# Kernel tuning notes

Measured on AMD Instinct MI355X. Metric: run time of the kernel, lower is better.

The kernel has to match this reference:

```python
import jax, jax.numpy as jnp
import numpy as np

B, S, H = 2, 2048, 3584
NH, NKV, HD = 28, 4, 128
GROUPS = NH // NKV  # 7
SCALING = HD ** -0.5
NEG = -1e9


def setup_inputs() -> dict:
    key = jax.random.key(0)
    ks = jax.random.split(key, 10)
    hidden_states = jax.random.normal(ks[0], (B, S, H), jnp.float32)
    # RoPE tables (faithful functional form; use real rotary angles)
    inv_freq = 1.0 / (1000000.0 ** (jnp.arange(0, HD, 2, dtype=jnp.float32) / HD))
    pos = jnp.arange(S, dtype=jnp.float32)
    freqs = jnp.outer(pos, inv_freq)                 # [S, HD/2]
    emb = jnp.concatenate([freqs, freqs], axis=-1)   # [S, HD]
    cos = jnp.broadcast_to(jnp.cos(emb)[None], (B, S, HD))
    sin = jnp.broadcast_to(jnp.sin(emb)[None], (B, S, HD))
    # additive causal mask [1,1,S,S]
    causal = jnp.tril(jnp.ones((S, S), dtype=bool))
    attention_mask = jnp.where(causal, 0.0, NEG).astype(jnp.float32)[None, None]
    sc = 0.02
    Wq = jax.random.normal(ks[1], (NH * HD, H), jnp.float32) * sc
    bq = jax.random.normal(ks[2], (NH * HD,), jnp.float32) * sc
    Wk = jax.random.normal(ks[3], (NKV * HD, H), jnp.float32) * sc
    bk = jax.random.normal(ks[4], (NKV * HD,), jnp.float32) * sc
    Wv = jax.random.normal(ks[5], (NKV * HD, H), jnp.float32) * sc
    bv = jax.random.normal(ks[6], (NKV * HD,), jnp.float32) * sc
    Wo = jax.random.normal(ks[7], (H, NH * HD), jnp.float32) * sc
    return dict(hidden_states=hidden_states, cos=cos, sin=sin,
                attention_mask=attention_mask, Wq=Wq, bq=bq, Wk=Wk, bk=bk,
                Wv=Wv, bv=bv, Wo=Wo)


def _rotate_half(x):
    x1, x2 = jnp.split(x, 2, axis=-1)
    return jnp.concatenate([-x2, x1], axis=-1)


def reference(hidden_states, cos, sin, attention_mask, Wq, bq, Wk, bk, Wv, bv, Wo):
    Bv_, Sv_ = hidden_states.shape[:2]
    # projections -> [B, heads, S, HD]
    q = (hidden_states @ Wq.T + bq).reshape(Bv_, Sv_, NH, HD).transpose(0, 2, 1, 3)
    k = (hidden_states @ Wk.T + bk).reshape(Bv_, Sv_, NKV, HD).transpose(0, 2, 1, 3)
    v = (hidden_states @ Wv.T + bv).reshape(Bv_, Sv_, NKV, HD).transpose(0, 2, 1, 3)
    # RoPE (unsqueeze_dim=1)
    c, s = cos[:, None], sin[:, None]
    q = q * c + _rotate_half(q) * s
    k = k * c + _rotate_half(k) * s
    # repeat_kv for GQA
    k = jnp.repeat(k, GROUPS, axis=1)  # [B, NH, S, HD]
    v = jnp.repeat(v, GROUPS, axis=1)
    scores = jnp.einsum('bhqd,bhkd->bhqk', q, k) * SCALING
    scores = scores + attention_mask[:, :, :, :k.shape[-2]]
    probs = jax.nn.softmax(scores.astype(jnp.float32), axis=-1).astype(q.dtype)
    attn = jnp.einsum('bhqk,bhkd->bhqd', probs, v)          # [B, NH, S, HD]
    attn = attn.transpose(0, 2, 1, 3).reshape(Bv_, Sv_, NH * HD)
    out = attn @ Wo.T
    return out, probs
```

## Files before the change

kernel.cpp:

```cpp
#include <hip/hip_runtime.h>

#define Bn 2
#define Sn 2048
#define Hn 3584
#define NHn 28
#define NKVn 4
#define HDn 128
#define GROUPSn 7
#define SCALEF 0.08838834764831845f
#define SCALE2F (0.08838834764831845f * 1.4426950408889634f)
#define NOUT 14680064LL

typedef __attribute__((ext_vector_type(4))) float f4v;
typedef __attribute__((ext_vector_type(16))) float f32x16;
typedef __attribute__((ext_vector_type(8))) short bf16x8;
typedef __attribute__((ext_vector_type(4))) short s16x4;

typedef __attribute__((address_space(1))) void gvoid;
typedef __attribute__((address_space(3))) void lvoid;
#define GLL16(g, l) __builtin_amdgcn_global_load_lds((gvoid*)(void*)(g), (lvoid*)(l), 16, 0, 0)

__device__ __forceinline__ short f2bf(float f) {
  unsigned u = __builtin_bit_cast(unsigned, f);
  u = (u + 0x7fffu + ((u >> 16) & 1u)) >> 16;
  return (short)u;
}

__global__ __launch_bounds__(256) void cast_bf16(const float* __restrict__ in,
                                                 short* __restrict__ out, long long n4) {
  long long i = (long long)blockIdx.x * 256 + threadIdx.x;
  long long stride = (long long)gridDim.x * 256;
  for (; i < n4; i += stride) {
    f4v f = ((const f4v*)in)[i];
    s16x4 o = { f2bf(f.x), f2bf(f.y), f2bf(f.z), f2bf(f.w) };
    ((s16x4*)out)[i] = o;
  }
}

__global__ __launch_bounds__(256) void cast_weights(const float* __restrict__ Wq,
                                                    const float* __restrict__ Wk,
                                                    const float* __restrict__ Wv,
                                                    const float* __restrict__ Wo,
                                                    short* __restrict__ wqkv_bf,
                                                    short* __restrict__ wo_bf) {
  long long i = (long long)blockIdx.x * 256 + threadIdx.x;
  long long stride = (long long)gridDim.x * 256;
  for (; i < 7340032LL; i += stride) {
    const f4v* src;
    s16x4* dst;
    if (i < 3211264LL) {
      src = (const f4v*)Wq + i;             dst = (s16x4*)wqkv_bf + i;
    } else if (i < 3670016LL) {
      src = (const f4v*)Wk + (i - 3211264); dst = (s16x4*)(wqkv_bf + 12845056LL) + (i - 3211264);
    } else if (i < 4128768LL) {
      src = (const f4v*)Wv + (i - 3670016); dst = (s16x4*)(wqkv_bf + 14680064LL) + (i - 3670016);
    } else {
      src = (const f4v*)Wo + (i - 4128768); dst = (s16x4*)wo_bf + (i - 4128768);
    }
    f4v f = *src;
    s16x4 o = { f2bf(f.x), f2bf(f.y), f2bf(f.z), f2bf(f.w) };
    *dst = o;
  }
}

__global__ __launch_bounds__(256) void concat_bias(const float* __restrict__ bq,
                                                   const float* __restrict__ bk,
                                                   const float* __restrict__ bv,
                                                   float* __restrict__ out) {
  int i = blockIdx.x * 256 + threadIdx.x;
  if (i < 3584) out[i] = bq[i];
  else if (i < 4096) out[i] = bk[i - 3584];
  else if (i < 4608) out[i] = bv[i - 4096];
}

__device__ __forceinline__ void mm128x64_core(const short* __restrict__ Atile, long long lda,
                                              const short* __restrict__ Btile, long long ldb,
                                              int nk, short* lA, short* lB, f4v (&acc)[4][4]) {
  const int tid = threadIdx.x;
  const int lane = tid & 63;
  const int wr = (tid >> 6) >> 1, wc = (tid >> 6) & 1;
  const int fr = lane & 15;
  const int g = lane >> 4;
  int rsw[4], csw[4];
#pragma unroll
  for (int i = 0; i < 4; ++i) {
    int M = i * 256 + tid;
    rsw[i] = M >> 3;
    csw[i] = (M & 7) ^ (rsw[i] & 7);
  }
  for (int kt = 0; kt < nk; ++kt) {
#pragma unroll
    for (int i = 0; i < 4; ++i) {
      GLL16(Atile + (long long)rsw[i] * lda + kt * 64 + csw[i] * 8, lA + (i * 256 + tid) * 8);
      GLL16(Btile + (long long)rsw[i] * ldb + kt * 64 + csw[i] * 8, lB + (i * 256 + tid) * 8);
    }
    __syncthreads();
#pragma unroll
    for (int kk = 0; kk < 2; ++kk) {
      bf16x8 af[4], bf[4];
#pragma unroll
      for (int m = 0; m < 4; ++m) {
        int r = wr * 64 + m * 16 + fr;
        af[m] = *(const bf16x8*)&lA[r * 64 + ((kk * 4 + g) ^ (r & 7)) * 8];
      }
#pragma unroll
      for (int n = 0; n < 4; ++n) {
        int r = wc * 64 + n * 16 + fr;
        bf[n] = *(const bf16x8*)&lB[r * 64 + ((kk * 4 + g) ^ (r & 7)) * 8];
      }
#pragma unroll
      for (int m = 0; m < 4; ++m)
#pragma unroll
        for (int n = 0; n < 4; ++n)
          acc[m][n] = __builtin_amdgcn_mfma_f32_16x16x32_bf16(af[m], bf[n], acc[m][n], 0, 0, 0);
    }
    __syncthreads();
  }
}

__global__ __launch_bounds__(256) void gemm_persist(const short* __restrict__ A,
                                                    const short* __restrict__ B,
                                                    float* __restrict__ C,
                                                    const float* __restrict__ bias,
                                                    int K, int N, int gx, int ntiles) {
  __shared__ alignas(16) short lA[8192];
  __shared__ alignas(16) short lB[8192];
  const int nt8 = ntiles >> 3;
  const int lane = threadIdx.x & 63;
  const int wr = (threadIdx.x >> 6) >> 1, wc = (threadIdx.x >> 6) & 1;
  const int rr = (lane >> 4) * 4, cc = lane & 15;
  for (int vt = blockIdx.x; vt < ntiles; vt += gridDim.x) {
    const int tile = (vt & 7) * nt8 + (vt >> 3);
    const int bx = tile % gx, by = tile / gx;
    const long long brow = (long long)by * 128;
    const long long bcol = (long long)bx * 128;
    f4v acc[4][4] = {};
    mm128x64_core(A + brow * K, K, B + bcol * K, K, K >> 6, lA, lB, acc);
#pragma unroll
    for (int n = 0; n < 4; ++n) {
      long long col = bcol + wc * 64 + n * 16 + cc;
      float bv = bias ? bias[col] : 0.f;
#pragma unroll
      for (int m = 0; m < 4; ++m) {
#pragma unroll
        for (int j = 0; j < 4; ++j) {
          long long row = brow + wr * 64 + m * 16 + rr + j;
          C[row * N + col] = acc[m][n][j] + bv;
        }
      }
    }
  }
}

__global__ __launch_bounds__(256) void rope_qk(const float* __restrict__ qkv,
                                               const float* __restrict__ cosb,
                                               const float* __restrict__ sinb,
                                               short* __restrict__ qo,
                                               short* __restrict__ ko) {
  long long bs = blockIdx.x;
  int b = (int)(bs >> 11);
  int s = (int)(bs & 2047);
  const float* row = qkv + bs * 4608;
  const float* cp = cosb + bs * 128;
  const float* sp = sinb + bs * 128;
  for (int i = threadIdx.x; i < 4096; i += 256) {
    int d = i & 127;
    float c = cp[d], sn = sp[d];
    float x = row[i];
    float xr = (d < 64) ? -row[i + 64] : row[i - 64];
    short v = f2bf(x * c + xr * sn);
    if (i < 3584) {
      int h = i >> 7;
      qo[(((long long)(b * NHn + h) * Sn + s)) * HDn + d] = v;
    } else {
      int h = (i - 3584) >> 7;
      ko[(((long long)(b * NKVn + h) * Sn + s)) * HDn + d] = v;
    }
  }
}

__global__ void vtrans(const float* __restrict__ qkv, short* __restrict__ vt) {
  __shared__ float tile[32][33];
  int bh = blockIdx.z;
  int b = bh >> 2, h = bh & 3;
  int s0 = blockIdx.x * 32, d0 = blockIdx.y * 32;
  int tx = threadIdx.x, ty = threadIdx.y;
#pragma unroll
  for (int j = 0; j < 32; j += 8) {
    int s = s0 + ty + j;
    tile[ty + j][tx] = qkv[((long long)(b * Sn + s)) * 4608 + 4096 + h * 128 + d0 + tx];
  }
  __syncthreads();
#pragma unroll
  for (int j = 0; j < 32; j += 8) {
    int d = d0 + ty + j;
    vt[((long long)(bh * 128 + d)) * Sn + s0 + tx] = f2bf(tile[tx][ty + j]);
  }
}

__global__ __launch_bounds__(256, 1) void fused_attn7(const short* __restrict__ Q,
                                                      const short* __restrict__ Kb,
                                                      const short* __restrict__ Vt,
                                                      float* __restrict__ probs,
                                                      short* __restrict__ attn) {
  __shared__ alignas(16) short lK[2][8192];
  __shared__ alignas(16) short lV[8192];
  const int tid = threadIdx.x;
  const int w = tid >> 6;
  const int lane = tid & 63;
  const int lam = lane & 31, h = lane >> 5;
  const int qb = 15 - (int)blockIdx.x;
  const int bh = blockIdx.y;
  const int b = bh / NHn, hh = bh - b * NHn, kv = hh / GROUPSn;
  const short* Qb = Q + (long long)bh * (Sn * HDn);
  const short* Kbb = Kb + (long long)(b * NKVn + kv) * (Sn * HDn);
  const short* Vb = Vt + (long long)(b * NKVn + kv) * (HDn * Sn);
  float* Pb = probs + (long long)bh * ((long long)Sn * Sn) + (long long)qb * 128 * Sn;
  const int qloc = w * 32 + lam;

  bf16x8 qf[8];
  {
    const short* qr = Qb + (long long)(qb * 128 + qloc) * HDn + h * 8;
#pragma unroll
    for (int s = 0; s < 8; ++s) qf[s] = *(const bf16x8*)(qr + s * 16);
  }
  int rswK[4], cswK[4];
#pragma unroll
  for (int i = 0; i < 4; ++i) {
    int M = i * 256 + tid;
    rswK[i] = M >> 4;
    cswK[i] = (M & 15) ^ (rswK[i] & 15);
  }
  int rswV[4], cswV[4];
#pragma unroll
  for (int i = 0; i < 4; ++i) {
    int M = i * 256 + tid;
    rswV[i] = M >> 3;
    cswV[i] = (M & 7) ^ (rswV[i] & 7);
  }
  const int c8 = lam & 15;
  const int v8 = lam & 7;
  const int nkt = 2 * qb + 2;

#define STAGEK(BUF, KT) do {                                                      \
    const short* base_ = Kbb + (long long)(KT) * 64 * HDn;                        \
    _Pragma("unroll")                                                             \
    for (int i = 0; i < 4; ++i)                                                   \
      GLL16(base_ + (long long)rswK[i] * HDn + cswK[i] * 8,                       \
            (short*)lK[BUF] + (i * 256 + tid) * 8);                               \
  } while (0)

#define STAGEV(KT) do {                                                           \
    _Pragma("unroll")                                                             \
    for (int i = 0; i < 4; ++i)                                                   \
      GLL16(Vb + (long long)rswV[i] * Sn + (KT) * 64 + cswV[i] * 8,               \
            lV + (i * 256 + tid) * 8);                                            \
  } while (0)

#define QKT2(ACCP, LCUR) do {                                                     \
    __builtin_amdgcn_s_setprio(1);                                                \
    _Pragma("unroll")                                                             \
    for (int s = 0; s < 8; ++s) {                                                 \
      const int co_ = ((s * 2 + h) ^ c8) * 8;                                     \
      _Pragma("unroll")                                                           \
      for (int a = 0; a < 2; ++a) {                                               \
        bf16x8 kf_ = *(const bf16x8*)&(LCUR)[(a * 32 + lam) * 128 + co_];         \
        ACCP[a] = __builtin_amdgcn_mfma_f32_32x32x16_bf16(kf_, qf[s], ACCP[a], 0, 0, 0); \
      }                                                                           \
    }                                                                             \
    __builtin_amdgcn_s_setprio(0);                                                \
  } while (0)

  float lsum = 0.f;
  STAGEK(0, 0);
  int cur = 0;
  for (int kt = 0; kt < nkt; ++kt) {
    __syncthreads();
    if (kt + 1 < nkt) STAGEK(cur ^ 1, kt + 1);
    const short* lcur = (const short*)lK[cur];
    f32x16 accp[2] = {};
    QKT2(accp, lcur);
    const int kbase = kt * 64 - qb * 128;
#pragma unroll
    for (int a = 0; a < 2; ++a)
#pragma unroll
      for (int r = 0; r < 16; ++r) {
        int kloc = a * 32 + (r & 3) + 8 * (r >> 2) + 4 * h;
        float s = fminf(accp[a][r] * SCALE2F, 86.5f);
        float p = exp2f(s);
        if (kbase + kloc > qloc) p = 0.f;
        lsum += p;
      }
    cur ^= 1;
  }
  lsum += __shfl_xor(lsum, 32);
  const float invl = 1.f / lsum;

  __syncthreads();
  STAGEK(0, 0);
  cur = 0;
  f32x16 acco[4] = {};
  for (int kt = 0; kt < nkt; ++kt) {
    __syncthreads();
    STAGEV(kt);
    const short* lcur = (const short*)lK[cur];
    f32x16 accp[2] = {};
    QKT2(accp, lcur);
    __syncthreads();
    if (kt + 1 < nkt) STAGEK(cur ^ 1, kt + 1);
    const int kbase = kt * 64 - qb * 128;
    float* prow = Pb + (long long)qloc * Sn + kt * 64 + 4 * h;
#pragma unroll
    for (int a = 0; a < 2; ++a) {
      float pn[16];
#pragma unroll
      for (int r = 0; r < 16; ++r) {
        int kloc = a * 32 + (r & 3) + 8 * (r >> 2) + 4 * h;
        float s = fminf(accp[a][r] * SCALE2F, 86.5f);
        float p = exp2f(s) * invl;
        if (kbase + kloc > qloc) p = 0.f;
        pn[r] = p;
      }
#pragma unroll
      for (int T = 0; T < 4; ++T) {
        f4v v = { pn[4 * T], pn[4 * T + 1], pn[4 * T + 2], pn[4 * T + 3] };
        *(f4v*)(prow + a * 32 + 8 * T) = v;
      }
#pragma unroll
      for (int ci = 0; ci < 2; ++ci) {
        const int ro = ci * 8;
        float r0 = __shfl_xor(h ? pn[ro + 0] : pn[ro + 4], 32);
        float r1 = __shfl_xor(h ? pn[ro + 1] : pn[ro + 5], 32);
        float r2 = __shfl_xor(h ? pn[ro + 2] : pn[ro + 6], 32);
        float r3 = __shfl_xor(h ? pn[ro + 3] : pn[ro + 7], 32);
        float t0 = h ? r0 : pn[ro + 0];
        float t1 = h ? r1 : pn[ro + 1];
        float t2 = h ? r2 : pn[ro + 2];
        float t3 = h ? r3 : pn[ro + 3];
        float t4 = h ? pn[ro + 4] : r0;
        float t5 = h ? pn[ro + 5] : r1;
        float t6 = h ? pn[ro + 6] : r2;
        float t7 = h ? pn[ro + 7] : r3;
        bf16x8 pf = { f2bf(t0), f2bf(t1), f2bf(t2), f2bf(t3),
                      f2bf(t4), f2bf(t5), f2bf(t6), f2bf(t7) };
        const int c = a * 2 + ci;
        __builtin_amdgcn_s_setprio(1);
#pragma unroll
        for (int f = 0; f < 4; ++f) {
          bf16x8 vf = *(const bf16x8*)&lV[(f * 32 + lam) * 64 + ((c * 2 + h) ^ v8) * 8];
          acco[f] = __builtin_amdgcn_mfma_f32_32x32x16_bf16(pf, vf, acco[f], 0, 0, 0);
        }
        __builtin_amdgcn_s_setprio(0);
      }
    }
    cur ^= 1;
  }
#undef QKT2
#undef STAGEV
#undef STAGEK

#pragma unroll
  for (int f = 0; f < 4; ++f)
#pragma unroll
    for (int r = 0; r < 16; ++r) {
      int qv = (r & 3) + 8 * (r >> 2) + 4 * h;
      long long q = (long long)qb * 128 + w * 32 + qv;
      attn[((long long)(b * Sn) + q) * Hn + hh * HDn + f * 32 + lam] = f2bf(acco[f][r]);
    }

  {
    const int r0 = tid >> 3;
    const int c0 = tid & 7;
    f4v z = {0.f, 0.f, 0.f, 0.f};
    for (int ct = qb + 1; ct < 16; ++ct) {
      float* base = Pb + (long long)ct * 128;
#pragma unroll
      for (int rr = 0; rr < 128; rr += 32) {
        f4v* rowp = (f4v*)(base + (long long)(r0 + rr) * Sn);
#pragma unroll
        for (int c = 0; c < 4; ++c) __builtin_nontemporal_store(z, &rowp[c0 + c * 8]);
      }
    }
  }
}


extern "C" void kernel_launch(void* const* d_in, const int* in_sizes, int n_in,
                              void* d_out, int out_size, void* d_ws, size_t ws_size,
                              hipStream_t stream) {
  const float* hs   = (const float*)d_in[0];
  const float* cosb = (const float*)d_in[1];
  const float* sinb = (const float*)d_in[2];
  const float* Wq = (const float*)d_in[4];
  const float* bq = (const float*)d_in[5];
  const float* Wk = (const float*)d_in[6];
  const float* bk = (const float*)d_in[7];
  const float* Wv = (const float*)d_in[8];
  const float* bv = (const float*)d_in[9];
  const float* Wo = (const float*)d_in[10];
  float* out   = (float*)d_out;
  float* probs = out + NOUT;
  char* ws = (char*)d_ws;
  short* hs_bf   = (short*)(ws + 0);
  short* attn_bf = hs_bf;
  short* wqkv_bf = (short*)(ws + 29360128LL);
  short* q_bf    = wqkv_bf;
  short* wo_bf   = (short*)(ws + 62390272LL);
  float* bias_qkv= (float*)(ws + 88080384LL);
  float* qkv     = (float*)(ws + 88098816LL);
  short* k_bf    = (short*)(ws + 163596288LL);
  short* vt_bf   = (short*)(ws + 167790592LL);

  cast_bf16<<<2048, 256, 0, stream>>>(hs, hs_bf, 3670016LL);
  cast_weights<<<2048, 256, 0, stream>>>(Wq, Wk, Wv, Wo, wqkv_bf, wo_bf);
  concat_bias<<<18, 256, 0, stream>>>(bq, bk, bv, bias_qkv);

  gemm_persist<<<768, 256, 0, stream>>>(hs_bf, wqkv_bf, qkv, bias_qkv, 3584, 4608, 36, 1152);

  rope_qk<<<4096, 256, 0, stream>>>(qkv, cosb, sinb, q_bf, k_bf);
  vtrans<<<dim3(64, 4, 8), dim3(32, 8), 0, stream>>>(qkv, vt_bf);

  fused_attn7<<<dim3(16, 56), 256, 0, stream>>>(q_bf, k_bf, vt_bf, probs, attn_bf);

  gemm_persist<<<768, 256, 0, stream>>>(attn_bf, wo_bf, out, nullptr, 3584, 3584, 28, 896);
}
```

Before: 875.4 us.

## Triple-buffer GEMM LDS tiles with async prefetch and K-step of 32

```diff
diff --git a/kernel.cpp b/kernel.cpp
--- a/kernel.cpp
+++ b/kernel.cpp
@@ -73,49 +73,55 @@
   else if (i < 4608) out[i] = bv[i - 4096];
 }
 
-__device__ __forceinline__ void mm128x64_core(const short* __restrict__ Atile, long long lda,
-                                              const short* __restrict__ Btile, long long ldb,
-                                              int nk, short* lA, short* lB, f4v (&acc)[4][4]) {
+__device__ __forceinline__ void mm128_pipe(const short* __restrict__ Atile, long long lda,
+                                           const short* __restrict__ Btile, long long ldb,
+                                           int nk, short (*lA)[4096], short (*lB)[4096],
+                                           f4v (&acc)[4][4]) {
   const int tid = threadIdx.x;
   const int lane = tid & 63;
   const int wr = (tid >> 6) >> 1, wc = (tid >> 6) & 1;
+  const int srow = tid >> 2;
+  const int scol = (tid & 3) * 8;
+  const short* a0 = Atile + (long long)srow * lda + scol;
+  const short* a1 = Atile + (long long)(srow + 64) * lda + scol;
+  const short* b0 = Btile + (long long)srow * ldb + scol;
+  const short* b1 = Btile + (long long)(srow + 64) * ldb + scol;
   const int fr = lane & 15;
-  const int g = lane >> 4;
-  int rsw[4], csw[4];
-#pragma unroll
-  for (int i = 0; i < 4; ++i) {
-    int M = i * 256 + tid;
-    rsw[i] = M >> 3;
-    csw[i] = (M & 7) ^ (rsw[i] & 7);
-  }
+  const int kc = (lane >> 4) * 8;
+#define STG(BUF, KT) do {                                        \
+    GLL16(a0 + (KT) * 32, lA[BUF] + tid * 8);                    \
+    GLL16(a1 + (KT) * 32, lA[BUF] + (256 + tid) * 8);            \
+    GLL16(b0 + (KT) * 32, lB[BUF] + tid * 8);                    \
+    GLL16(b1 + (KT) * 32, lB[BUF] + (256 + tid) * 8);            \
+  } while (0)
+  STG(0, 0);
+  if (nk > 1) STG(1, 1);
   for (int kt = 0; kt < nk; ++kt) {
-#pragma unroll
-    for (int i = 0; i < 4; ++i) {
-      GLL16(Atile + (long long)rsw[i] * lda + kt * 64 + csw[i] * 8, lA + (i * 256 + tid) * 8);
-      GLL16(Btile + (long long)rsw[i] * ldb + kt * 64 + csw[i] * 8, lB + (i * 256 + tid) * 8);
-    }
-    __syncthreads();
-#pragma unroll
-    for (int kk = 0; kk < 2; ++kk) {
-      bf16x8 af[4], bf[4];
-#pragma unroll
-      for (int m = 0; m < 4; ++m) {
-        int r = wr * 64 + m * 16 + fr;
-        af[m] = *(const bf16x8*)&lA[r * 64 + ((kk * 4 + g) ^ (r & 7)) * 8];
-      }
-#pragma unroll
-      for (int n = 0; n < 4; ++n) {
-        int r = wc * 64 + n * 16 + fr;
-        bf[n] = *(const bf16x8*)&lB[r * 64 + ((kk * 4 + g) ^ (r & 7)) * 8];
-      }
-#pragma unroll
-      for (int m = 0; m < 4; ++m)
-#pragma unroll
-        for (int n = 0; n < 4; ++n)
-          acc[m][n] = __builtin_amdgcn_mfma_f32_16x16x32_bf16(af[m], bf[n], acc[m][n], 0, 0, 0);
-    }
-    __syncthreads();
-  }
+    if (kt + 1 < nk) {
+      asm volatile("s_waitcnt vmcnt(4)" ::: "memory");
+    } else {
+      asm volatile("s_waitcnt vmcnt(0)" ::: "memory");
+    }
+    __builtin_amdgcn_s_barrier();
+    __builtin_amdgcn_sched_barrier(0);
+    if (kt + 2 < nk) STG((kt + 2) % 3, kt + 2);
+    const short* cA = lA[kt % 3];
+    const short* cB = lB[kt % 3];
+    bf16x8 af[4], bf[4];
+#pragma unroll
+    for (int m = 0; m < 4; ++m)
+      af[m] = *(const bf16x8*)&cA[(wr * 64 + m * 16 + fr) * 32 + kc];
+#pragma unroll
+    for (int n = 0; n < 4; ++n)
+      bf[n] = *(const bf16x8*)&cB[(wc * 64 + n * 16 + fr) * 32 + kc];
+#pragma unroll
+    for (int m = 0; m < 4; ++m)
+#pragma unroll
+      for (int n = 0; n < 4; ++n)
+        acc[m][n] = __builtin_amdgcn_mfma_f32_16x16x32_bf16(af[m], bf[n], acc[m][n], 0, 0, 0);
+  }
+#undef STG
+  __syncthreads();
 }
 
 __global__ __launch_bounds__(256) void gemm_persist(const short* __restrict__ A,
@@ -123,8 +129,8 @@
                                                     float* __restrict__ C,
                                                     const float* __restrict__ bias,
                                                     int K, int N, int gx, int ntiles) {
-  __shared__ alignas(16) short lA[8192];
-  __shared__ alignas(16) short lB[8192];
+  __shared__ alignas(16) short lA[3][4096];
+  __shared__ alignas(16) short lB[3][4096];
   const int nt8 = ntiles >> 3;
   const int lane = threadIdx.x & 63;
   const int wr = (threadIdx.x >> 6) >> 1, wc = (threadIdx.x >> 6) & 1;
@@ -135,7 +141,7 @@
     const long long brow = (long long)by * 128;
     const long long bcol = (long long)bx * 128;
     f4v acc[4][4] = {};
-    mm128x64_core(A + brow * K, K, B + bcol * K, K, K >> 6, lA, lB, acc);
+    mm128_pipe(A + brow * K, K, B + bcol * K, K, K >> 5, lA, lB, acc);
 #pragma unroll
     for (int n = 0; n < 4; ++n) {
       long long col = bcol + wc * 64 + n * 16 + cc;
```

New measurement: 945.3 us. 1.08x slower.
